# Kernel tuning notes

Measured on AMD Instinct MI355X. Metric: run time of the kernel, lower is better.

The kernel has to match this reference:

```python
import jax, jax.numpy as jnp
import numpy as np

DIM = 512
HEADS = 8
DIM_HEAD = 64
HIDDEN = HEADS * DIM_HEAD  # 512
B, H, W = 32, 64, 64


def setup_inputs() -> dict:
    key = jax.random.key(0)
    k1, k2, k3 = jax.random.split(key, 3)
    x = jax.random.normal(k1, (B, H, W, DIM), dtype=jnp.float32)
    w_qkv = jax.random.normal(k2, (DIM, 3 * HIDDEN), dtype=jnp.float32) * 0.02
    w_out = jax.random.normal(k3, (HIDDEN, DIM), dtype=jnp.float32) * 0.02
    b_out = jnp.zeros((DIM,), dtype=jnp.float32)
    return {"x": x, "w_qkv": w_qkv, "w_out": w_out, "b_out": b_out}


def reference(x, w_qkv, w_out, b_out):
    b, h, w, c = x.shape
    n = h * w
    scale = DIM_HEAD ** (-0.5)
    # 1x1 conv (no bias) == matmul over channels
    qkv = jnp.einsum('bhwc,cf->bhwf', x, w_qkv)  # (b, h, w, 3*hidden)
    q, k, v = jnp.split(qkv, 3, axis=-1)
    # 'b x y (h c) -> b (x y) h c'
    def to_heads(t):
        return t.reshape(b, n, HEADS, DIM_HEAD)
    q, k, v = map(to_heads, (q, k, v))
    q = q * scale
    # contraction over spatial axis d=(x*y): sim (b, dim_head_i, heads, dim_head_j)
    sim = jnp.einsum('bdhi,bdhj->bihj', q, k)
    sim = sim - jnp.max(sim, axis=-1, keepdims=True)
    attn = jax.nn.softmax(sim, axis=-1)
    out = jnp.einsum('bihj,bdhj->bdhi', attn, v)  # (b, n, heads, dim_head)
    out = out.reshape(b, h, w, HIDDEN)
    # output 1x1 conv with bias
    return jnp.einsum('bhwf,fc->bhwc', out, w_out) + b_out
```

## Files before the change

### kernel.cpp

```cpp
#include <hip/hip_runtime.h>
#include <hip/hip_bf16.h>
#include <stdint.h>

using bf16x8 = __attribute__((ext_vector_type(8))) __bf16;
using s16x8  = __attribute__((ext_vector_type(8))) short;
using f32x4  = __attribute__((ext_vector_type(4))) float;

__device__ __forceinline__ uint16_t f2bf(float f) {
    uint32_t u = __builtin_bit_cast(uint32_t, f);
    u += 0x7fffu + ((u >> 16) & 1u);
    return (uint16_t)(u >> 16);
}
__device__ __forceinline__ float bf2f(uint16_t h) {
    return __builtin_bit_cast(float, (uint32_t)h << 16);
}

__device__ __forceinline__ void async16(uint16_t* lds_dst, const uint16_t* g_src) {
    __builtin_amdgcn_global_load_lds(
        (const __attribute__((address_space(1))) void*)g_src,
        (__attribute__((address_space(3))) void*)lds_dst,
        16, 0, 0);
}

__global__ void wprep_k(const float* __restrict__ in, uint16_t* __restrict__ out,
                        int ld_in, int col0, float scale, int ldo, int dup) {
    int idx = blockIdx.x * 256 + threadIdx.x;
    int co = idx >> 9, r = idx & 511;
    uint16_t v = f2bf(in[r * ld_in + col0 + co] * scale);
    out[co * ldo + r] = v;
    if (dup) out[co * ldo + 512 + r] = v;
}

__global__ void wconv_k(const float* __restrict__ in, uint16_t* __restrict__ out) {
    int idx = blockIdx.x * 256 + threadIdx.x;
    int k = idx >> 9, c = idx & 511;
    out[k * 512 + c] = f2bf(in[k * 1536 + 1024 + c]);
}

__global__ __launch_bounds__(256, 4)
void xt_k(const float* __restrict__ x, uint16_t* __restrict__ xb, uint16_t* __restrict__ xT)
{
    __shared__ uint16_t lt[64 * 68];
    const int tid = threadIdx.x;
    const int bi = blockIdx.x;
    const int b = bi >> 9;
    const int rem = bi & 511;
    const int st = rem >> 3, ct = rem & 7;
    const int c4 = (tid & 15) * 4;
#pragma unroll
    for (int rep = 0; rep < 4; ++rep) {
        int r = (tid >> 4) + rep * 16;
        long gs = (long)(b * 4096 + st * 64 + r) * 512 + ct * 64 + c4;
        float4 v = *(const float4*)(x + gs);
        uint16_t t[4];
        t[0] = f2bf(v.x); t[1] = f2bf(v.y); t[2] = f2bf(v.z); t[3] = f2bf(v.w);
        *(ushort4*)(xb + gs) = *(const ushort4*)t;
#pragma unroll
        for (int q = 0; q < 4; ++q) lt[r * 68 + c4 + q] = t[q];
    }
    __syncthreads();
    const int s4 = (tid & 15) * 4;
#pragma unroll
    for (int rep = 0; rep < 4; ++rep) {
        int c = (tid >> 4) + rep * 16;
        uint16_t t[4];
#pragma unroll
        for (int q = 0; q < 4; ++q) t[q] = lt[(s4 + q) * 68 + c];
        *(ushort4*)(xT + (long)(b * 512 + ct * 64 + c) * 4096 + st * 64 + s4) =
            *(const ushort4*)t;
    }
}

template<bool OUTF32>
__global__ __launch_bounds__(512, 2)
void g8_k(const uint16_t* __restrict__ A, const uint16_t* __restrict__ Bt,
          void* __restrict__ Cp, const float* __restrict__ bias,
          int K, int lda, int ldb, int ldc, int mtiles, int ntiles,
          long abr, long bbe, long cbr)
{
    __shared__ uint16_t lds[65536];
    const int tid  = threadIdx.x;
    const int lane = tid & 63;
    const int wv   = tid >> 6;
    const int wr   = wv >> 2, wc = wv & 3;

    const int q8 = gridDim.x >> 3;
    const int l  = (blockIdx.x & 7) * q8 + (blockIdx.x >> 3);
    const int per   = mtiles * ntiles;
    const int batch = l / per;
    const int rem   = l - batch * per;
    const int mt    = rem / ntiles, nt = rem - mt * ntiles;

    const long arow0 = abr * batch + (long)mt * 256;
    const uint16_t* abase = A + arow0 * (long)lda;
    const uint16_t* btb   = Bt + bbe * batch + (long)nt * 256 * ldb;

    const int fr = lane & 15;
    const int cx0 = (((0 << 2) | (lane >> 4)) ^ (fr & 7)) * 8;
    const int cx1 = (((1 << 2) | (lane >> 4)) ^ (fr & 7)) * 8;
    const int baseA = wr * 8192 + fr * 64;
    const int baseB = (2 + (wc >> 1)) * 8192 + ((wc & 1) * 64 + fr) * 64;

    const int NT = K >> 6;

    auto stage = [&](int slot, const uint16_t* gb, int rstride, int k0) {
#pragma unroll
        for (int i = 0; i < 2; ++i) {
            int si = i * 512 + wv * 64 + lane;
            int rr = si >> 3, cc = (si & 7) ^ (rr & 7);
            async16(&lds[slot * 8192 + (i * 512 + wv * 64) * 8],
                    gb + (long)rr * rstride + k0 + cc * 8);
        }
    };

    f32x4 acc[8][4];
#pragma unroll
    for (int m = 0; m < 8; ++m)
#pragma unroll
        for (int n = 0; n < 4; ++n) acc[m][n] = (f32x4){0.f, 0.f, 0.f, 0.f};

    bf16x8 af[4], bfq[4];

    auto rdA = [&](int mb, int b4, int cx) {
#pragma unroll
        for (int mi = 0; mi < 4; ++mi)
            af[mi] = __builtin_bit_cast(bf16x8,
                *(const s16x8*)&lds[b4 * 8192 + baseA + (mb + mi) * 1024 + cx]);
    };
    auto rdB = [&](int b4, int cx) {
#pragma unroll
        for (int n = 0; n < 4; ++n)
            bfq[n] = __builtin_bit_cast(bf16x8,
                *(const s16x8*)&lds[b4 * 8192 + baseB + n * 1024 + cx]);
    };
    auto mm = [&](int mb) {
        asm volatile("s_waitcnt lgkmcnt(0)" ::: "memory");
        __builtin_amdgcn_sched_barrier(0);
        __builtin_amdgcn_s_setprio(1);
#pragma unroll
        for (int mi = 0; mi < 4; ++mi)
#pragma unroll
            for (int n = 0; n < 4; ++n)
                acc[mb + mi][n] = __builtin_amdgcn_mfma_f32_16x16x32_bf16(
                    af[mi], bfq[n], acc[mb + mi][n], 0, 0, 0);
        __builtin_amdgcn_s_setprio(0);
        __builtin_amdgcn_s_barrier();
    };

    stage(0, abase,              lda, 0);
    stage(1, abase + 128L * lda, lda, 0);
    stage(2, btb,                ldb, 0);
    stage(3, btb + 128L * ldb,   ldb, 0);
    stage(6, btb,                ldb, 64);
    stage(7, btb + 128L * ldb,   ldb, 64);
    asm volatile("s_waitcnt vmcnt(4)" ::: "memory");
    __builtin_amdgcn_sched_barrier(0);
    __builtin_amdgcn_s_barrier();

    for (int it = 0; it < (NT >> 1); ++it) {
        const int E = 2 * it, Od = E + 1;
        const bool s3 = (E + 2) < NT;
        const bool s7 = (Od + 2) < NT;
        const int kE2 = (E + 2) << 6, kO1 = Od << 6, kO2 = (Od + 2) << 6;

        rdB(0, cx0); rdA(0, 0, cx0);
        stage(4, abase,              lda, kO1);
        stage(5, abase + 128L * lda, lda, kO1);
        __builtin_amdgcn_s_barrier();
        mm(0);
        rdA(4, 0, cx0);
        __builtin_amdgcn_s_barrier();
        mm(4);
        rdB(0, cx1); rdA(0, 0, cx1);
        __builtin_amdgcn_s_barrier();
        mm(0);
        rdA(4, 0, cx1);
        if (s3) {
            stage(2, btb,              ldb, kE2);
            stage(3, btb + 128L * ldb, ldb, kE2);
            asm volatile("s_waitcnt vmcnt(4)" ::: "memory");
        } else {
            asm volatile("s_waitcnt vmcnt(0)" ::: "memory");
        }
        __builtin_amdgcn_sched_barrier(0);
        __builtin_amdgcn_s_barrier();
        mm(4);
        rdB(4, cx0); rdA(0, 4, cx0);
        if (s3) {
            stage(0, abase,              lda, kE2);
            stage(1, abase + 128L * lda, lda, kE2);
        }
        __builtin_amdgcn_s_barrier();
        mm(0);
        rdA(4, 4, cx0);
        __builtin_amdgcn_s_barrier();
        mm(4);
        rdB(4, cx1); rdA(0, 4, cx1);
        __builtin_amdgcn_s_barrier();
        mm(0);
        rdA(4, 4, cx1);
        if (s7) {
            stage(6, btb,              ldb, kO2);
            stage(7, btb + 128L * ldb, ldb, kO2);
            asm volatile("s_waitcnt vmcnt(4)" ::: "memory");
        } else {
            asm volatile("s_waitcnt vmcnt(0)" ::: "memory");
        }
        __builtin_amdgcn_sched_barrier(0);
        __builtin_amdgcn_s_barrier();
        mm(4);
    }

    const long crow0 = cbr * batch + (long)mt * 256 + wr * 128;
    const int  col0  = nt * 256 + wc * 64;
    float bv[4];
#pragma unroll
    for (int n = 0; n < 4; ++n)
        bv[n] = bias ? bias[col0 + n * 16 + (lane & 15)] : 0.f;
#pragma unroll
    for (int m = 0; m < 8; ++m) {
#pragma unroll
        for (int r = 0; r < 4; ++r) {
            long row = crow0 + m * 16 + (lane >> 4) * 4 + r;
#pragma unroll
            for (int n = 0; n < 4; ++n) {
                int col = col0 + n * 16 + (lane & 15);
                float v = acc[m][n][r];
                if constexpr (OUTF32)
                    ((float*)Cp)[row * (long)ldc + col] = v + bv[n];
                else
                    ((uint16_t*)Cp)[row * (long)ldc + col] = f2bf(v);
            }
        }
    }
}

__global__ __launch_bounds__(512, 2)
void g8G_k(const uint16_t* __restrict__ X, uint16_t* __restrict__ Gcat)
{
    __shared__ uint16_t lds[65536];
    const int tid  = threadIdx.x;
    const int lane = tid & 63;
    const int wv   = tid >> 6;
    const int wr   = wv >> 2, wc = wv & 3;

    const int q8 = gridDim.x >> 3;
    const int l  = (blockIdx.x & 7) * q8 + (blockIdx.x >> 3);
    const int bz = l >> 2;
    const int rem = l & 3;
    const int mt = rem >> 1, nt = rem & 1;
    const int b = bz >> 1, z = bz & 1;

    const uint16_t* xb0 = X + (long)b * 512 * 4096 + z * 2048;
    const uint16_t* abase = xb0 + (long)mt * 256 * 4096;
    const uint16_t* btb   = xb0 + (long)nt * 256 * 4096;

    const int fr = lane & 15;
    const int cx0 = (((0 << 2) | (lane >> 4)) ^ (fr & 7)) * 8;
    const int cx1 = (((1 << 2) | (lane >> 4)) ^ (fr & 7)) * 8;
    const int baseA = wr * 8192 + fr * 64;
    const int baseB = (2 + (wc >> 1)) * 8192 + ((wc & 1) * 64 + fr) * 64;

    const int NT = 32;

    auto stage = [&](int slot, const uint16_t* gb, int k0) {
#pragma unroll
        for (int i = 0; i < 2; ++i) {
            int si = i * 512 + wv * 64 + lane;
            int rr = si >> 3, cc = (si & 7) ^ (rr & 7);
            async16(&lds[slot * 8192 + (i * 512 + wv * 64) * 8],
                    gb + (long)rr * 4096 + k0 + cc * 8);
        }
    };

    f32x4 acc[8][4];
#pragma unroll
    for (int m = 0; m < 8; ++m)
#pragma unroll
        for (int n = 0; n < 4; ++n) acc[m][n] = (f32x4){0.f, 0.f, 0.f, 0.f};

    bf16x8 af[4], bfq[4];
    auto rdA = [&](int mb, int b4, int cx) {
#pragma unroll
        for (int mi = 0; mi < 4; ++mi)
            af[mi] = __builtin_bit_cast(bf16x8,
                *(const s16x8*)&lds[b4 * 8192 + baseA + (mb + mi) * 1024 + cx]);
    };
    auto rdB = [&](int b4, int cx) {
#pragma unroll
        for (int n = 0; n < 4; ++n)
            bfq[n] = __builtin_bit_cast(bf16x8,
                *(const s16x8*)&lds[b4 * 8192 + baseB + n * 1024 + cx]);
    };
    auto mm = [&](int mb) {
        asm volatile("s_waitcnt lgkmcnt(0)" ::: "memory");
        __builtin_amdgcn_sched_barrier(0);
        __builtin_amdgcn_s_setprio(1);
#pragma unroll
        for (int mi = 0; mi < 4; ++mi)
#pragma unroll
            for (int n = 0; n < 4; ++n)
                acc[mb + mi][n] = __builtin_amdgcn_mfma_f32_16x16x32_bf16(
                    af[mi], bfq[n], acc[mb + mi][n], 0, 0, 0);
        __builtin_amdgcn_s_setprio(0);
        __builtin_amdgcn_s_barrier();
    };

    stage(0, abase,               0);
    stage(1, abase + 128L * 4096, 0);
    stage(2, btb,                 0);
    stage(3, btb + 128L * 4096,   0);
    stage(6, btb,                 64);
    stage(7, btb + 128L * 4096,   64);
    asm volatile("s_waitcnt vmcnt(4)" ::: "memory");
    __builtin_amdgcn_sched_barrier(0);
    __builtin_amdgcn_s_barrier();

    for (int it = 0; it < (NT >> 1); ++it) {
        const int E = 2 * it, Od = E + 1;
        const bool s3 = (E + 2) < NT;
        const bool s7 = (Od + 2) < NT;
        const int kE2 = (E + 2) << 6, kO1 = Od << 6, kO2 = (Od + 2) << 6;

        rdB(0, cx0); rdA(0, 0, cx0);
        stage(4, abase,               kO1);
        stage(5, abase + 128L * 4096, kO1);
        __builtin_amdgcn_s_barrier();
        mm(0);
        rdA(4, 0, cx0);
        __builtin_amdgcn_s_barrier();
        mm(4);
        rdB(0, cx1); rdA(0, 0, cx1);
        __builtin_amdgcn_s_barrier();
        mm(0);
        rdA(4, 0, cx1);
        if (s3) {
            stage(2, btb,               kE2);
            stage(3, btb + 128L * 4096, kE2);
            asm volatile("s_waitcnt vmcnt(4)" ::: "memory");
        } else {
            asm volatile("s_waitcnt vmcnt(0)" ::: "memory");
        }
        __builtin_amdgcn_sched_barrier(0);
        __builtin_amdgcn_s_barrier();
        mm(4);
        rdB(4, cx0); rdA(0, 4, cx0);
        if (s3) {
            stage(0, abase,               kE2);
            stage(1, abase + 128L * 4096, kE2);
        }
        __builtin_amdgcn_s_barrier();
        mm(0);
        rdA(4, 4, cx0);
        __builtin_amdgcn_s_barrier();
        mm(4);
        rdB(4, cx1); rdA(0, 4, cx1);
        __builtin_amdgcn_s_barrier();
        mm(0);
        rdA(4, 4, cx1);
        if (s7) {
            stage(6, btb,               kO2);
            stage(7, btb + 128L * 4096, kO2);
            asm volatile("s_waitcnt vmcnt(4)" ::: "memory");
        } else {
            asm volatile("s_waitcnt vmcnt(0)" ::: "memory");
        }
        __builtin_amdgcn_sched_barrier(0);
        __builtin_amdgcn_s_barrier();
        mm(4);
    }

    uint16_t* o = Gcat + (long)b * 524288;
    const int row0 = mt * 256 + wr * 128;
    const int col0 = z * 512 + nt * 256 + wc * 64;
#pragma unroll
    for (int m = 0; m < 8; ++m)
#pragma unroll
        for (int r = 0; r < 4; ++r) {
            int row = row0 + m * 16 + (lane >> 4) * 4 + r;
#pragma unroll
            for (int n = 0; n < 4; ++n)
                o[(long)row * 1024 + col0 + n * 16 + (lane & 15)] = f2bf(acc[m][n][r]);
        }
}

__global__ __launch_bounds__(512, 1)
void simfull_k(const uint16_t* __restrict__ Gcat, const uint16_t* __restrict__ wkTcat,
               const uint16_t* __restrict__ wqTs, uint16_t* __restrict__ attnT)
{
    __shared__ uint16_t sm[73728];
    const int tid  = threadIdx.x;
    const int lane = tid & 63;
    const int wv   = tid >> 6;
    const int fr   = lane & 15;
    const int bi = blockIdx.x;
    const int h = bi >> 5;
    const int b = (bi & 7) * 4 + ((bi >> 3) & 3);

    const uint16_t* gb  = Gcat + (long)b * 524288;
    const uint16_t* ab  = wkTcat + (long)h * 64 * 1024;
    const uint16_t* qb2 = wqTs + (long)h * 64 * 512;

    f32x4 acc[4][4];
#pragma unroll
    for (int mf = 0; mf < 4; ++mf)
#pragma unroll
        for (int nf = 0; nf < 4; ++nf) acc[mf][nf] = (f32x4){0.f, 0.f, 0.f, 0.f};

    for (int t = 0; t < 16; ++t) {
        const int k0 = t * 64;
#pragma unroll
        for (int i = 0; i < 8; ++i) {
            int si = i * 64 + lane;
            int rr = si >> 3, cc = (si & 7) ^ (rr & 7);
            async16(&sm[wv * 4096 + i * 512],
                    gb + (long)(wv * 64 + rr) * 1024 + k0 + cc * 8);
        }
        {
            int rr = wv * 8 + (lane >> 3);
            int cc = (lane & 7) ^ (rr & 7);
            async16(&sm[32768 + wv * 512],
                    ab + (long)rr * 1024 + k0 + cc * 8);
        }
        asm volatile("s_waitcnt vmcnt(0)" ::: "memory");
        __syncthreads();
#pragma unroll
        for (int ks = 0; ks < 2; ++ks) {
            bf16x8 af[4], bfq[4];
            int cx = ((ks * 4 + (lane >> 4)) ^ (fr & 7)) * 8;
#pragma unroll
            for (int mf = 0; mf < 4; ++mf)
                af[mf] = __builtin_bit_cast(bf16x8,
                    *(const s16x8*)&sm[32768 + (mf * 16 + fr) * 64 + cx]);
#pragma unroll
            for (int nf = 0; nf < 4; ++nf)
                bfq[nf] = __builtin_bit_cast(bf16x8,
                    *(const s16x8*)&sm[(wv * 64 + nf * 16 + fr) * 64 + cx]);
#pragma unroll
            for (int mf = 0; mf < 4; ++mf)
#pragma unroll
                for (int nf = 0; nf < 4; ++nf)
                    acc[mf][nf] = __builtin_amdgcn_mfma_f32_16x16x32_bf16(
                        af[mf], bfq[nf], acc[mf][nf], 0, 0, 0);
        }
        __syncthreads();
    }

#pragma unroll
    for (int mf = 0; mf < 4; ++mf)
#pragma unroll
        for (int nf = 0; nf < 4; ++nf)
#pragma unroll
            for (int r = 0; r < 4; ++r) {
                int j = mf * 16 + (lane >> 4) * 4 + r;
                int c = wv * 64 + nf * 16 + fr;
                float v = acc[mf][nf][r];
                uint16_t hi = f2bf(v);
                int off = j * 512 + ((c >> 3) ^ (j & 7)) * 8 + (c & 7);
                sm[off] = hi;
                sm[32768 + off] = f2bf(v - bf2f(hi));
            }
    __syncthreads();

    f32x4 a2[4][4];
#pragma unroll
    for (int mf = 0; mf < 4; ++mf)
#pragma unroll
        for (int nf = 0; nf < 4; ++nf) a2[mf][nf] = (f32x4){0.f, 0.f, 0.f, 0.f};
#pragma unroll
    for (int ks = 0; ks < 2; ++ks) {
        bf16x8 af[4], bh[4], bl[4];
#pragma unroll
        for (int mf = 0; mf < 4; ++mf)
            af[mf] = __builtin_bit_cast(bf16x8,
                *(const s16x8*)&qb2[(long)(mf * 16 + fr) * 512 + wv * 64 + ks * 32 + (lane >> 4) * 8]);
#pragma unroll
        for (int nf = 0; nf < 4; ++nf) {
            int j = nf * 16 + fr;
            int ch = (wv * 8 + ks * 4 + (lane >> 4)) ^ (fr & 7);
            bh[nf] = __builtin_bit_cast(bf16x8, *(const s16x8*)&sm[j * 512 + ch * 8]);
            bl[nf] = __builtin_bit_cast(bf16x8, *(const s16x8*)&sm[32768 + j * 512 + ch * 8]);
        }
#pragma unroll
        for (int mf = 0; mf < 4; ++mf)
#pragma unroll
            for (int nf = 0; nf < 4; ++nf) {
                a2[mf][nf] = __builtin_amdgcn_mfma_f32_16x16x32_bf16(
                    af[mf], bh[nf], a2[mf][nf], 0, 0, 0);
                a2[mf][nf] = __builtin_amdgcn_mfma_f32_16x16x32_bf16(
                    af[mf], bl[nf], a2[mf][nf], 0, 0, 0);
            }
    }

    float* red = (float*)&sm[65536];
    for (int w = 0; w < 8; ++w) {
        if (wv == w) {
#pragma unroll
            for (int mf = 0; mf < 4; ++mf)
#pragma unroll
                for (int nf = 0; nf < 4; ++nf)
#pragma unroll
                    for (int r = 0; r < 4; ++r) {
                        int i = mf * 16 + (lane >> 4) * 4 + r;
                        int j = nf * 16 + fr;
                        float* p = &red[i * 64 + j];
                        *p = (w == 0) ? a2[mf][nf][r] : (*p + a2[mf][nf][r]);
                    }
        }
        __syncthreads();
    }

    float* rt1 = (float*)&sm[0];
    float* rt2 = (float*)&sm[512];
    const int i = tid >> 2, jc = tid & 3;
    float s[16];
    if (tid < 256) {
#pragma unroll
        for (int jj = 0; jj < 16; ++jj) s[jj] = red[i * 64 + jc * 16 + jj];
        float mx = s[0];
#pragma unroll
        for (int jj = 1; jj < 16; ++jj) mx = fmaxf(mx, s[jj]);
        rt1[i * 4 + jc] = mx;
    }
    __syncthreads();
    if (tid < 256) {
        float m4 = fmaxf(fmaxf(rt1[i * 4], rt1[i * 4 + 1]),
                         fmaxf(rt1[i * 4 + 2], rt1[i * 4 + 3]));
        float sum = 0.f;
#pragma unroll
        for (int jj = 0; jj < 16; ++jj) { s[jj] = __expf(s[jj] - m4); sum += s[jj]; }
        rt2[i * 4 + jc] = sum;
    }
    __syncthreads();
    if (tid < 256) {
        float tot = rt2[i * 4] + rt2[i * 4 + 1] + rt2[i * 4 + 2] + rt2[i * 4 + 3];
        float inv = 1.f / tot;
        uint16_t* at = attnT + (long)(b * 8 + h) * 4096;
#pragma unroll
        for (int jj = 0; jj < 16; ++jj)
            at[(jc * 16 + jj) * 64 + i] = f2bf(s[jj] * inv);
    }
}

__global__ __launch_bounds__(256, 1)
void w2_k(const uint16_t* __restrict__ attnT, const uint16_t* __restrict__ woutT,
          uint16_t* __restrict__ W2T)
{
    const int tid = threadIdx.x;
    const int lane = tid & 63, wv = tid >> 6;
    const int b = blockIdx.x >> 3, h = blockIdx.x & 7;
    const uint16_t* at = attnT + (long)blockIdx.x * 4096;

    bf16x8 bfrag[2][4];
#pragma unroll
    for (int ks = 0; ks < 2; ++ks)
#pragma unroll
        for (int nf = 0; nf < 4; ++nf) {
            s16x8 v = *(const s16x8*)&at[(nf * 16 + (lane & 15)) * 64 + ks * 32 + (lane >> 4) * 8];
            bfrag[ks][nf] = __builtin_bit_cast(bf16x8, v);
        }
    f32x4 acc[8][4];
#pragma unroll
    for (int mf = 0; mf < 8; ++mf)
#pragma unroll
        for (int nf = 0; nf < 4; ++nf) acc[mf][nf] = (f32x4){0.f, 0.f, 0.f, 0.f};
#pragma unroll
    for (int mf = 0; mf < 8; ++mf) {
        int c = wv * 128 + mf * 16 + (lane & 15);
#pragma unroll
        for (int ks = 0; ks < 2; ++ks) {
            s16x8 v = *(const s16x8*)&woutT[(long)c * 512 + h * 64 + ks * 32 + (lane >> 4) * 8];
            bf16x8 af = __builtin_bit_cast(bf16x8, v);
#pragma unroll
            for (int nf = 0; nf < 4; ++nf)
                acc[mf][nf] = __builtin_amdgcn_mfma_f32_16x16x32_bf16(
                    af, bfrag[ks][nf], acc[mf][nf], 0, 0, 0);
        }
    }
    uint16_t* o = W2T + (long)b * 512 * 512;
#pragma unroll
    for (int mf = 0; mf < 8; ++mf)
#pragma unroll
        for (int nf = 0; nf < 4; ++nf)
#pragma unroll
            for (int r = 0; r < 4; ++r) {
                int c = wv * 128 + mf * 16 + (lane >> 4) * 4 + r;
                int j = nf * 16 + (lane & 15);
                o[(long)c * 512 + h * 64 + j] = f2bf(acc[mf][nf][r]);
            }
}

extern "C" void kernel_launch(void* const* d_in, const int* in_sizes, int n_in,
                              void* d_out, int out_size, void* d_ws, size_t ws_size,
                              hipStream_t stream)
{
    const float* x     = (const float*)d_in[0];
    const float* w_qkv = (const float*)d_in[1];
    const float* w_out = (const float*)d_in[2];
    const float* b_out = (const float*)d_in[3];
    float* out = (float*)d_out;

    char* ws = (char*)d_ws;
    uint16_t* xb     = (uint16_t*)(ws);
    uint16_t* xT     = (uint16_t*)(ws + 134217728L);
    uint16_t* Gcat   = (uint16_t*)(ws + 268435456L);
    uint16_t* attnT  = (uint16_t*)(ws + 301989888L);
    uint16_t* W2T    = (uint16_t*)(ws + 304087040L);
    uint16_t* Bteff  = (uint16_t*)(ws + 320864256L);
    uint16_t* wqTs   = (uint16_t*)(ws + 354418688L);
    uint16_t* wkTcat = (uint16_t*)(ws + 354942976L);
    uint16_t* woutT  = (uint16_t*)(ws + 355991552L);
    uint16_t* wv_rm  = (uint16_t*)(ws + 356515840L);

    wprep_k<<<1024, 256, 0, stream>>>(w_qkv, wqTs, 1536, 0, 0.125f, 512, 0);
    wprep_k<<<1024, 256, 0, stream>>>(w_qkv, wkTcat, 1536, 512, 1.f, 1024, 1);
    wprep_k<<<1024, 256, 0, stream>>>(w_out, woutT, 512, 0, 1.f, 512, 0);
    wconv_k<<<1024, 256, 0, stream>>>(w_qkv, wv_rm);

    xt_k<<<16384, 256, 0, stream>>>(x, xb, xT);

    g8G_k<<<256, 512, 0, stream>>>(xT, Gcat);

    simfull_k<<<256, 512, 0, stream>>>(Gcat, wkTcat, wqTs, attnT);

    w2_k<<<256, 256, 0, stream>>>(attnT, woutT, W2T);

    g8_k<false><<<128, 512, 0, stream>>>(
        W2T, wv_rm, Bteff, nullptr,
        512, 512, 512, 512, 2, 2, 512L, 0L, 512L);

    g8_k<true><<<1024, 512, 0, stream>>>(
        xb, Bteff, out, b_out,
        512, 512, 512, 512, 16, 2, 4096L, 262144L, 4096L);
}
```

Baseline: 382.1 us.

## Exploit Gram matrix symmetry and merge weight-prep kernels into one launch

The per-batch Gram matrix X^T X is symmetric, so the off-diagonal (mt=1,nt=0) tile is no longer computed. The (0,1) tile's block also writes its transpose, cutting the Gram kernel from 256 to 192 blocks. The four weight conversion kernels are fused into a single launch indexed by section, removing three launch overheads. The transposed store uses 8-byte scattered writes with a strided column pattern, which may be poorly coalesced. With 192 blocks on 256 CUs, fewer CUs are in use.

```diff
diff --git a/kernel.cpp b/kernel.cpp
--- a/kernel.cpp
+++ b/kernel.cpp
@@ -22,19 +22,24 @@
         16, 0, 0);
 }
 
-__global__ void wprep_k(const float* __restrict__ in, uint16_t* __restrict__ out,
-                        int ld_in, int col0, float scale, int ldo, int dup) {
-    int idx = blockIdx.x * 256 + threadIdx.x;
+__global__ void wprep_all(const float* __restrict__ wqkv, const float* __restrict__ wout,
+                          uint16_t* __restrict__ wqTs, uint16_t* __restrict__ wkTcat,
+                          uint16_t* __restrict__ woutT, uint16_t* __restrict__ wv_rm)
+{
+    int sec = blockIdx.x >> 10;
+    int idx = (blockIdx.x & 1023) * 256 + threadIdx.x;
     int co = idx >> 9, r = idx & 511;
-    uint16_t v = f2bf(in[r * ld_in + col0 + co] * scale);
-    out[co * ldo + r] = v;
-    if (dup) out[co * ldo + 512 + r] = v;
-}
-
-__global__ void wconv_k(const float* __restrict__ in, uint16_t* __restrict__ out) {
-    int idx = blockIdx.x * 256 + threadIdx.x;
-    int k = idx >> 9, c = idx & 511;
-    out[k * 512 + c] = f2bf(in[k * 1536 + 1024 + c]);
+    if (sec == 0) {
+        wqTs[co * 512 + r] = f2bf(wqkv[r * 1536 + co] * 0.125f);
+    } else if (sec == 1) {
+        uint16_t v = f2bf(wqkv[r * 1536 + 512 + co]);
+        wkTcat[co * 1024 + r] = v;
+        wkTcat[co * 1024 + 512 + r] = v;
+    } else if (sec == 2) {
+        woutT[co * 512 + r] = f2bf(wout[r * 512 + co]);
+    } else {
+        wv_rm[co * 512 + r] = f2bf(wqkv[co * 1536 + 1024 + r]);
+    }
 }
 
 __global__ __launch_bounds__(256, 4)
@@ -246,10 +251,11 @@
 
     const int q8 = gridDim.x >> 3;
     const int l  = (blockIdx.x & 7) * q8 + (blockIdx.x >> 3);
-    const int bz = l >> 2;
-    const int rem = l & 3;
-    const int mt = rem >> 1, nt = rem & 1;
-    const int b = bz >> 1, z = bz & 1;
+    const int g  = l / 3;
+    const int quad = l - g * 3;
+    const int b = g >> 1, z = g & 1;
+    const int mt = (quad == 1) ? 1 : 0;
+    const int nt = (quad == 0) ? 0 : 1;
 
     const uint16_t* xb0 = X + (long)b * 512 * 4096 + z * 2048;
     const uint16_t* abase = xb0 + (long)mt * 256 * 4096;
@@ -371,17 +377,30 @@
     }
 
     uint16_t* o = Gcat + (long)b * 524288;
+    const int zoff = z * 512;
     const int row0 = mt * 256 + wr * 128;
-    const int col0 = z * 512 + nt * 256 + wc * 64;
-#pragma unroll
-    for (int m = 0; m < 8; ++m)
+    const int col0 = nt * 256 + wc * 64;
+#pragma unroll
+    for (int m = 0; m < 8; ++m) {
 #pragma unroll
         for (int r = 0; r < 4; ++r) {
             int row = row0 + m * 16 + (lane >> 4) * 4 + r;
 #pragma unroll
             for (int n = 0; n < 4; ++n)
-                o[(long)row * 1024 + col0 + n * 16 + (lane & 15)] = f2bf(acc[m][n][r]);
-        }
+                o[(long)row * 1024 + zoff + col0 + n * 16 + (lane & 15)] = f2bf(acc[m][n][r]);
+        }
+        if (quad == 2) {
+            int rbase = row0 + m * 16 + (lane >> 4) * 4;
+#pragma unroll
+            for (int n = 0; n < 4; ++n) {
+                int col = col0 + n * 16 + (lane & 15);
+                uint16_t t[4];
+#pragma unroll
+                for (int r = 0; r < 4; ++r) t[r] = f2bf(acc[m][n][r]);
+                *(ushort4*)&o[(long)col * 1024 + zoff + rbase] = *(const ushort4*)t;
+            }
+        }
+    }
 }
 
 __global__ __launch_bounds__(512, 1)
@@ -612,14 +631,11 @@
     uint16_t* woutT  = (uint16_t*)(ws + 355991552L);
     uint16_t* wv_rm  = (uint16_t*)(ws + 356515840L);
 
-    wprep_k<<<1024, 256, 0, stream>>>(w_qkv, wqTs, 1536, 0, 0.125f, 512, 0);
-    wprep_k<<<1024, 256, 0, stream>>>(w_qkv, wkTcat, 1536, 512, 1.f, 1024, 1);
-    wprep_k<<<1024, 256, 0, stream>>>(w_out, woutT, 512, 0, 1.f, 512, 0);
-    wconv_k<<<1024, 256, 0, stream>>>(w_qkv, wv_rm);
+    wprep_all<<<4096, 256, 0, stream>>>(w_qkv, w_out, wqTs, wkTcat, woutT, wv_rm);
 
     xt_k<<<16384, 256, 0, stream>>>(x, xb, xT);
 
-    g8G_k<<<256, 512, 0, stream>>>(xT, Gcat);
+    g8G_k<<<192, 512, 0, stream>>>(xT, Gcat);
 
     simfull_k<<<256, 512, 0, stream>>>(Gcat, wkTcat, wqTs, attnT);
 
```

New measurement: 378.8 us, median of 2. Within noise of the previous version (-0.9%).
